# Performance work log

Measured on AMD Instinct MI355X. Metric: run time of the kernel, lower is better.

## Reference

```python
import jax, jax.numpy as jnp
import numpy as np
from jax import lax

B, L, V, D, E, K, H, IMG = 256, 64, 32000, 1024, 8, 2, 512, 128


def setup_inputs() -> dict:
    key = jax.random.key(0)
    ks = jax.random.split(key, 24)
    n = lambda k, sh, s=0.02: (jax.random.normal(k, sh, jnp.float32) * s)
    return {
        "img": jax.random.normal(ks[0], (B, 3, IMG, IMG), jnp.float32),
        "tokens": jax.random.randint(ks[1], (B, L), 0, V),
        "mask": jnp.ones((B, L), jnp.int32),
        # image encoder convs (OIHW) + biases
        "cw1": n(ks[2], (32, 3, 3, 3)), "cb1": jnp.zeros((32,), jnp.float32),
        "cw2": n(ks[3], (64, 32, 3, 3)), "cb2": jnp.zeros((64,), jnp.float32),
        "cw3": n(ks[4], (128, 64, 3, 3)), "cb3": jnp.zeros((128,), jnp.float32),
        "cw4": n(ks[5], (256, 128, 3, 3)), "cb4": jnp.zeros((256,), jnp.float32),
        "enc_proj_w": n(ks[6], (256, D)), "enc_proj_b": jnp.zeros((D,), jnp.float32),
        # text encoder
        "embed": n(ks[7], (V, D)),
        # gate
        "gate_w": n(ks[8], (D, E)), "gate_b": jnp.zeros((E,), jnp.float32),
        # experts (stacked): y = relu(x@W1+b1)@W2+b2
        "exp_w1": n(ks[9], (E, D, H)), "exp_b1": jnp.zeros((E, H), jnp.float32),
        "exp_w2": n(ks[10], (E, H, D)), "exp_b2": jnp.zeros((E, D), jnp.float32),
        # contrastive projections (bias=False)
        "img_proj_w": n(ks[11], (D, D)),
        "txt_proj_w": n(ks[12], (D, D)),
        "logit_scale": jnp.log(jnp.float32(1.0 / 0.07)),
    }


def _conv(x, w, b, stride):
    y = lax.conv_general_dilated(x, w, (stride, stride), 'SAME',
                                 dimension_numbers=('NCHW', 'OIHW', 'NCHW'))
    return y + b[None, :, None, None]


def _img_encode(img, cw1, cb1, cw2, cb2, cw3, cb3, cw4, cb4, pw, pb):
    h = jax.nn.relu(_conv(img, cw1, cb1, 1))
    h = jax.nn.relu(_conv(h, cw2, cb2, 2))
    h = jax.nn.relu(_conv(h, cw3, cb3, 2))
    h = jax.nn.relu(_conv(h, cw4, cb4, 2))
    h = h.mean(axis=(2, 3))  # [B, 256]
    return h @ pw + pb


def _txt_encode(tokens, mask, embed):
    x = embed[tokens]                      # [B, L, D]
    m = mask[..., None].astype(jnp.float32)
    return (x * m).sum(axis=1) / jnp.maximum(m.sum(axis=1), 1.0)


def _moe(x, gate_w, gate_b, w1, b1, w2, b2):
    logits = x @ gate_w + gate_b                       # [B, E]
    probs = jax.nn.softmax(logits, axis=-1)
    topk_vals, topk_idx = lax.top_k(probs, K)
    w = topk_vals / (topk_vals.sum(axis=-1, keepdims=True) + 1e-9)  # [B, K]
    # dense expert compute (same math as the per-expert masked loop)
    h = jax.nn.relu(jnp.einsum('bd,edh->ebh', x, w1) + b1[:, None, :])
    y = jnp.einsum('ebh,ehd->ebd', h, w2) + b2[:, None, :]          # [E, B, D]
    y = jnp.transpose(y, (1, 0, 2))                                  # [B, E, D]
    sel = jnp.take_along_axis(y, topk_idx[:, :, None], axis=1)       # [B, K, D]
    out = (sel * w[:, :, None]).sum(axis=1)
    # F.kl_div(mean_probs.log(), uniform, reduction='batchmean')
    mp = probs.mean(axis=0)
    u = 1.0 / E
    aux = jnp.sum(u * (jnp.log(jnp.float32(u)) - jnp.log(mp))) / E
    return out, aux


def _normalize(x):
    return x / jnp.maximum(jnp.linalg.norm(x, axis=-1, keepdims=True), 1e-12)


def reference(img, tokens, mask, cw1, cb1, cw2, cb2, cw3, cb3, cw4, cb4,
              enc_proj_w, enc_proj_b, embed, gate_w, gate_b,
              exp_w1, exp_b1, exp_w2, exp_b2, img_proj_w, txt_proj_w, logit_scale):
    h_img = _img_encode(img, cw1, cb1, cw2, cb2, cw3, cb3, cw4, cb4, enc_proj_w, enc_proj_b)
    h_txt = _txt_encode(tokens, mask, embed)
    z_img, aux_img = _moe(h_img, gate_w, gate_b, exp_w1, exp_b1, exp_w2, exp_b2)
    z_txt, aux_txt = _moe(h_txt, gate_w, gate_b, exp_w1, exp_b1, exp_w2, exp_b2)
    e_img = _normalize(z_img @ img_proj_w)
    e_txt = _normalize(z_txt @ txt_proj_w)
    scale = jnp.minimum(jnp.exp(logit_scale), 100.0)
    logits_per_img = scale * (e_img @ e_txt.T)
    logits_per_txt = logits_per_img.T
    aux_loss = (aux_img + aux_txt) * 0.5
    return logits_per_img, logits_per_txt, aux_loss
```

## Files before the change

### kernel.cpp

```cpp
#include <hip/hip_runtime.h>
#include <hip/hip_bf16.h>
#include <math.h>

#define BATCH 256
#define CHUNK 32
#define NCHUNK (BATCH / CHUNK)
#define ECAP 256
#define NEXP 16

__global__ __launch_bounds__(256) void conv1_tiled(const float* __restrict__ in,
                                                   const float* __restrict__ w,
                                                   const float* __restrict__ bias,
                                                   float* __restrict__ out) {
  const int t = threadIdx.x;
  const int bc = blockIdx.x;
  const int quad = bc & 3;
  const int co = (bc >> 2) & 31;
  const int b = bc >> 7;
  const int tile = quad * 256 + t;
  const int tr = tile >> 4;
  const int tc = tile & 15;
  const int oh0 = tr * 2, ow0 = tc * 8;

  float wk[3][9];
#pragma unroll
  for (int ci = 0; ci < 3; ++ci)
#pragma unroll
    for (int k = 0; k < 9; ++k) wk[ci][k] = w[(co * 3 + ci) * 9 + k];

  const float bv = bias[co];
  float acc[2][8];
#pragma unroll
  for (int r = 0; r < 2; ++r)
#pragma unroll
    for (int c = 0; c < 8; ++c) acc[r][c] = bv;

  const float* __restrict__ ip = in + (size_t)b * 3 * 128 * 128;
#pragma unroll
  for (int ci = 0; ci < 3; ++ci) {
    const float* __restrict__ p = ip + ci * 128 * 128;
    float x[4][10];
#pragma unroll
    for (int r = 0; r < 4; ++r) {
      const int ih = oh0 - 1 + r;
      if (ih >= 0 && ih < 128) {
        const float* rowp = p + ih * 128 + ow0;
        x[r][0] = (ow0 > 0) ? rowp[-1] : 0.f;
        const float4 f0 = *(const float4*)(rowp);
        const float4 f1 = *(const float4*)(rowp + 4);
        x[r][1] = f0.x; x[r][2] = f0.y; x[r][3] = f0.z; x[r][4] = f0.w;
        x[r][5] = f1.x; x[r][6] = f1.y; x[r][7] = f1.z; x[r][8] = f1.w;
        x[r][9] = (ow0 + 8 < 128) ? rowp[8] : 0.f;
      } else {
#pragma unroll
        for (int q = 0; q < 10; ++q) x[r][q] = 0.f;
      }
    }
#pragma unroll
    for (int kh = 0; kh < 3; ++kh)
#pragma unroll
      for (int kw = 0; kw < 3; ++kw) {
        const float wv = wk[ci][kh * 3 + kw];
#pragma unroll
        for (int r = 0; r < 2; ++r)
#pragma unroll
          for (int c = 0; c < 8; ++c)
            acc[r][c] = fmaf(x[r + kh][c + kw], wv, acc[r][c]);
      }
  }
  float* __restrict__ op = out + (((size_t)b * 32 + co) * 128 + oh0) * 128 + ow0;
#pragma unroll
  for (int r = 0; r < 2; ++r)
#pragma unroll
    for (int c = 0; c < 8; ++c) op[r * 128 + c] = fmaxf(acc[r][c], 0.f);
}

template<int CIN, int HIN, int WIN, int HOUT, int WOUT, int COUT, int TH, int TW, int SLABS>
__global__ __launch_bounds__(256) void conv_s2_r4(const float* __restrict__ in,
                                                  const float* __restrict__ w,
                                                  const float* __restrict__ bias,
                                                  float* __restrict__ out) {
  constexpr int TPR = WOUT / TW;
  constexpr int TT = (HOUT / TH) * TPR;
  static_assert(TT == 64 * SLABS, "tile count mismatch");
  constexpr int GPI = (SLABS == 4) ? (COUT / 4) : (COUT / 16);
  const int wave = threadIdx.x >> 6;
  const int lane = threadIdx.x & 63;
  const int b = blockIdx.x / GPI;
  const int r = blockIdx.x % GPI;
  int cg, slab;
  if (SLABS == 4) { cg = r; slab = wave; }
  else           { cg = r * 4 + wave; slab = 0; }
  const int co0 = __builtin_amdgcn_readfirstlane(cg * 4);
  const int tile = slab * 64 + lane;
  const int tr = tile / TPR, tc = tile % TPR;
  const int oh0 = tr * TH, ow0 = tc * TW;
  const int ih0 = oh0 * 2, iw0 = ow0 * 2;

  const float* __restrict__ ip = in + (size_t)b * CIN * HIN * WIN + ih0 * WIN + iw0;
  const float* __restrict__ wp = w + (size_t)co0 * CIN * 9;

  float bv[4];
#pragma unroll
  for (int j = 0; j < 4; ++j) bv[j] = bias[co0 + j];
  float acc[4][TH][TW];
#pragma unroll
  for (int j = 0; j < 4; ++j)
#pragma unroll
    for (int rr = 0; rr < TH; ++rr)
#pragma unroll
      for (int c = 0; c < TW; ++c) acc[j][rr][c] = bv[j];

  for (int ci = 0; ci < CIN; ++ci) {
    float wk[4][9];
#pragma unroll
    for (int j = 0; j < 4; ++j)
#pragma unroll
      for (int k = 0; k < 9; ++k) wk[j][k] = wp[((size_t)j * CIN + ci) * 9 + k];

    float x[2 * TH + 1][2 * TW + 1];
    const float* __restrict__ rp = ip + (size_t)ci * HIN * WIN;
#pragma unroll
    for (int rr = 0; rr < 2 * TH + 1; ++rr) {
      const int ih = ih0 + rr;
      if (ih < HIN) {
        const float* rowp = rp + rr * WIN;
#pragma unroll
        for (int q = 0; q < (2 * TW) / 4; ++q) {
          const float4 f = *(const float4*)(rowp + q * 4);
          x[rr][q * 4 + 0] = f.x; x[rr][q * 4 + 1] = f.y;
          x[rr][q * 4 + 2] = f.z; x[rr][q * 4 + 3] = f.w;
        }
        x[rr][2 * TW] = (iw0 + 2 * TW < WIN) ? rowp[2 * TW] : 0.f;
      } else {
#pragma unroll
        for (int q = 0; q < 2 * TW + 1; ++q) x[rr][q] = 0.f;
      }
    }
#pragma unroll
    for (int kh = 0; kh < 3; ++kh)
#pragma unroll
      for (int kw = 0; kw < 3; ++kw) {
#pragma unroll
        for (int j = 0; j < 4; ++j) {
          const float wv = wk[j][kh * 3 + kw];
#pragma unroll
          for (int rr = 0; rr < TH; ++rr)
#pragma unroll
            for (int c = 0; c < TW; ++c)
              acc[j][rr][c] = fmaf(x[2 * rr + kh][2 * c + kw], wv, acc[j][rr][c]);
        }
      }
  }
#pragma unroll
  for (int j = 0; j < 4; ++j) {
    float* __restrict__ op = out + (((size_t)b * COUT + co0 + j) * HOUT + oh0) * WOUT + ow0;
#pragma unroll
    for (int rr = 0; rr < TH; ++rr)
#pragma unroll
      for (int c = 0; c < TW; ++c) op[rr * WOUT + c] = fmaxf(acc[j][rr][c], 0.f);
  }
}

__global__ __launch_bounds__(64) void pool_mean(const float* __restrict__ in,
                                                float* __restrict__ out) {
  const int bc = blockIdx.x;
  const float* p = in + (size_t)bc * 256;
  float s = p[threadIdx.x] + p[threadIdx.x + 64] + p[threadIdx.x + 128] + p[threadIdx.x + 192];
#pragma unroll
  for (int off = 32; off; off >>= 1) s += __shfl_down(s, off);
  if (threadIdx.x == 0) out[bc] = s * (1.f / 256.f);
}

__global__ __launch_bounds__(256) void enc_proj(const float* __restrict__ pooled,
                                                const float* __restrict__ W,
                                                const float* __restrict__ bias,
                                                float* __restrict__ out) {
  __shared__ float xs[256];
  const int b = blockIdx.x;
  const int t = threadIdx.x;
  xs[t] = pooled[b * 256 + t];
  __syncthreads();
#pragma unroll
  for (int dd = 0; dd < 4; ++dd) {
    const int d = t + dd * 256;
    float acc = bias[d];
    for (int i = 0; i < 256; ++i) acc = fmaf(xs[i], W[i * 1024 + d], acc);
    out[b * 1024 + d] = acc;
  }
}

__global__ __launch_bounds__(256) void txt_encode(const int* __restrict__ tokens,
                                                  const int* __restrict__ mask,
                                                  const float* __restrict__ embed,
                                                  float* __restrict__ out) {
  __shared__ int toks[64];
  __shared__ float ms[64];
  const int b = blockIdx.x;
  const int t = threadIdx.x;
  if (t < 64) {
    toks[t] = tokens[b * 64 + t];
    ms[t] = (float)mask[b * 64 + t];
  }
  __syncthreads();
  float denom = 0.f;
  for (int l = 0; l < 64; ++l) denom += ms[l];
  denom = fmaxf(denom, 1.f);
  const float inv = 1.f / denom;
#pragma unroll
  for (int dd = 0; dd < 4; ++dd) {
    const int d = t + dd * 256;
    float acc = 0.f;
    for (int l = 0; l < 64; ++l)
      acc = fmaf(embed[(size_t)toks[l] * 1024 + d], ms[l], acc);
    out[b * 1024 + d] = acc * inv;
  }
}

__global__ __launch_bounds__(64) void zero_cnt(int* __restrict__ cnt) {
  if (threadIdx.x < NEXP) cnt[threadIdx.x] = 0;
}

__global__ __launch_bounds__(256) void gate_topk(const float* __restrict__ x,
                                                 const float* __restrict__ gw,
                                                 const float* __restrict__ gb,
                                                 float* __restrict__ probs_out,
                                                 float* __restrict__ sel_w,
                                                 int* __restrict__ slot_of,
                                                 int* __restrict__ cnt,
                                                 int* __restrict__ slot_tok,
                                                 int emod_base) {
  const int b = blockIdx.x;
  __shared__ float part[256];
  __shared__ float logits[8];
  const int e = threadIdx.x & 7;
  const int ch = threadIdx.x >> 3;
  float acc = 0.f;
  for (int d = ch * 32; d < ch * 32 + 32; ++d)
    acc = fmaf(x[b * 1024 + d], gw[d * 8 + e], acc);
  part[threadIdx.x] = acc;
  __syncthreads();
  if (threadIdx.x < 8) {
    float s = gb[threadIdx.x];
    for (int c = 0; c < 32; ++c) s += part[c * 8 + threadIdx.x];
    logits[threadIdx.x] = s;
  }
  __syncthreads();
  if (threadIdx.x == 0) {
    float mx = logits[0];
    for (int i = 1; i < 8; ++i) mx = fmaxf(mx, logits[i]);
    float pe[8], sum = 0.f;
    for (int i = 0; i < 8; ++i) { pe[i] = expf(logits[i] - mx); sum += pe[i]; }
    const float inv = 1.f / sum;
    int i0 = 0;
    for (int i = 1; i < 8; ++i) if (pe[i] > pe[i0]) i0 = i;
    int i1 = (i0 == 0) ? 1 : 0;
    for (int i = 0; i < 8; ++i) { if (i == i0) continue; if (pe[i] > pe[i1]) i1 = i; }
    for (int i = 0; i < 8; ++i) probs_out[b * 8 + i] = pe[i] * inv;
    const float v0 = pe[i0] * inv, v1 = pe[i1] * inv;
    const float wsum = v0 + v1 + 1e-9f;
    const int sel[2] = {i0, i1};
    const float sw[2] = {v0 / wsum, v1 / wsum};
#pragma unroll
    for (int k = 0; k < 2; ++k) {
      const int ve = emod_base + sel[k];
      const int slot = atomicAdd(&cnt[ve], 1);
      slot_tok[ve * ECAP + slot] = b;
      slot_of[b * 2 + k] = ve * ECAP + slot;
      sel_w[b * 2 + k] = sw[k];
    }
  }
}

__global__ __launch_bounds__(256) void moe_ffn1(const float* __restrict__ h_img,
                                                const float* __restrict__ h_txt,
                                                const int* __restrict__ cnt,
                                                const int* __restrict__ slot_tok,
                                                const float* __restrict__ W1,
                                                const float* __restrict__ B1,
                                                float* __restrict__ hbuf) {
  const int ve = blockIdx.x >> 5;
  const int rem = blockIdx.x & 31;
  const int tchunk = rem >> 2;
  const int nchunk = rem & 3;
  const int tbase = tchunk * 32;
  const int scnt = cnt[ve];
  if (tbase >= scnt) return;
  const int n0 = nchunk * 128;
  const int e = ve & 7;
  const float* __restrict__ xsrc = (ve < 8) ? h_img : h_txt;
  const float* __restrict__ w1 = W1 + (size_t)e * 1024 * 512;

  __shared__ float xs[32][36];
  __shared__ float ws[32][128];

  const int tid = threadIdx.x;
  const int tokr = tid >> 3, kq = tid & 7;
  const int sidx = tbase + tokr;
  const int tok = (sidx < scnt) ? slot_tok[ve * ECAP + sidx] : 0;
  const int tn = tid & 31, tt = tid >> 5;
  const int n4 = tn * 4, t4 = tt * 4;

  float acc[4][4] = {};
  for (int k0 = 0; k0 < 1024; k0 += 32) {
    const float4 xv = *(const float4*)(xsrc + (size_t)tok * 1024 + k0 + kq * 4);
    float4 wv[4];
#pragma unroll
    for (int i = 0; i < 4; ++i) {
      const int idx = tid + i * 256;
      const int kk = idx >> 5, nq = idx & 31;
      wv[i] = *(const float4*)(w1 + (size_t)(k0 + kk) * 512 + n0 + nq * 4);
    }
    __syncthreads();
    xs[kq * 4 + 0][tokr] = xv.x; xs[kq * 4 + 1][tokr] = xv.y;
    xs[kq * 4 + 2][tokr] = xv.z; xs[kq * 4 + 3][tokr] = xv.w;
#pragma unroll
    for (int i = 0; i < 4; ++i) {
      const int idx = tid + i * 256;
      const int kk = idx >> 5, nq = idx & 31;
      *(float4*)&ws[kk][nq * 4] = wv[i];
    }
    __syncthreads();
#pragma unroll
    for (int k = 0; k < 32; ++k) {
      const float4 xr = *(const float4*)&xs[k][t4];
      const float4 wr = *(const float4*)&ws[k][n4];
      const float xa[4] = {xr.x, xr.y, xr.z, xr.w};
      const float wa[4] = {wr.x, wr.y, wr.z, wr.w};
#pragma unroll
      for (int ti = 0; ti < 4; ++ti)
#pragma unroll
        for (int ni = 0; ni < 4; ++ni)
          acc[ti][ni] = fmaf(xa[ti], wa[ni], acc[ti][ni]);
    }
  }
#pragma unroll
  for (int ti = 0; ti < 4; ++ti) {
    float* hp = hbuf + ((size_t)ve * ECAP + tbase + t4 + ti) * 512 + n0 + n4;
#pragma unroll
    for (int ni = 0; ni < 4; ++ni)
      hp[ni] = fmaxf(acc[ti][ni] + B1[e * 512 + n0 + n4 + ni], 0.f);
  }
}

__global__ __launch_bounds__(256) void moe_ffn2(const float* __restrict__ hbuf,
                                                const int* __restrict__ cnt,
                                                const float* __restrict__ W2,
                                                const float* __restrict__ B2,
                                                float* __restrict__ ybuf) {
  const int ve = blockIdx.x >> 6;
  const int rem = blockIdx.x & 63;
  const int tchunk = rem >> 3;
  const int nchunk = rem & 7;
  const int tbase = tchunk * 32;
  const int scnt = cnt[ve];
  if (tbase >= scnt) return;
  const int n0 = nchunk * 128;
  const int e = ve & 7;
  const float* __restrict__ w2 = W2 + (size_t)e * 512 * 1024;

  __shared__ float hs[32][36];
  __shared__ float ws[32][128];

  const int tid = threadIdx.x;
  const int tokr = tid >> 3, kq = tid & 7;
  const int tn = tid & 31, tt = tid >> 5;
  const int n4 = tn * 4, t4 = tt * 4;

  float acc[4][4] = {};
  for (int k0 = 0; k0 < 512; k0 += 32) {
    const float4 hv = *(const float4*)(hbuf + ((size_t)ve * ECAP + tbase + tokr) * 512 + k0 + kq * 4);
    float4 wv[4];
#pragma unroll
    for (int i = 0; i < 4; ++i) {
      const int idx = tid + i * 256;
      const int kk = idx >> 5, nq = idx & 31;
      wv[i] = *(const float4*)(w2 + (size_t)(k0 + kk) * 1024 + n0 + nq * 4);
    }
    __syncthreads();
    hs[kq * 4 + 0][tokr] = hv.x; hs[kq * 4 + 1][tokr] = hv.y;
    hs[kq * 4 + 2][tokr] = hv.z; hs[kq * 4 + 3][tokr] = hv.w;
#pragma unroll
    for (int i = 0; i < 4; ++i) {
      const int idx = tid + i * 256;
      const int kk = idx >> 5, nq = idx & 31;
      *(float4*)&ws[kk][nq * 4] = wv[i];
    }
    __syncthreads();
#pragma unroll
    for (int k = 0; k < 32; ++k) {
      const float4 xr = *(const float4*)&hs[k][t4];
      const float4 wr = *(const float4*)&ws[k][n4];
      const float xa[4] = {xr.x, xr.y, xr.z, xr.w};
      const float wa[4] = {wr.x, wr.y, wr.z, wr.w};
#pragma unroll
      for (int ti = 0; ti < 4; ++ti)
#pragma unroll
        for (int ni = 0; ni < 4; ++ni)
          acc[ti][ni] = fmaf(xa[ti], wa[ni], acc[ti][ni]);
    }
  }
#pragma unroll
  for (int ti = 0; ti < 4; ++ti) {
    float* yp = ybuf + ((size_t)ve * ECAP + tbase + t4 + ti) * 1024 + n0 + n4;
#pragma unroll
    for (int ni = 0; ni < 4; ++ni)
      yp[ni] = acc[ti][ni] + B2[e * 1024 + n0 + n4 + ni];
  }
}

__global__ __launch_bounds__(256) void moe_combine(const float* __restrict__ ybuf,
                                                   const int* __restrict__ slot_of,
                                                   const float* __restrict__ sel_w,
                                                   float* __restrict__ z_img,
                                                   float* __restrict__ z_txt) {
  const int bb = blockIdx.x;
  const int mod = bb >> 8;
  const int b = bb & 255;
  const int s0 = slot_of[bb * 2], s1 = slot_of[bb * 2 + 1];
  const float w0 = sel_w[bb * 2], w1 = sel_w[bb * 2 + 1];
  float* __restrict__ zp = (mod ? z_txt : z_img) + (size_t)b * 1024;
  const float* __restrict__ y0 = ybuf + (size_t)s0 * 1024;
  const float* __restrict__ y1 = ybuf + (size_t)s1 * 1024;
  const int t = threadIdx.x;
#pragma unroll
  for (int dd = 0; dd < 4; ++dd) {
    const int d = t + dd * 256;
    zp[d] = w0 * y0[d] + w1 * y1[d];
  }
}

__global__ __launch_bounds__(256) void proj_norm(const float* __restrict__ z,
                                                 const float* __restrict__ W,
                                                 float* __restrict__ e_out) {
  const int b = blockIdx.x;
  const int t = threadIdx.x;
  __shared__ float xs[1024];
  __shared__ float red[256];
#pragma unroll
  for (int i = 0; i < 4; ++i) xs[t + i * 256] = z[b * 1024 + t + i * 256];
  __syncthreads();
  float p[4];
  float ss = 0.f;
#pragma unroll
  for (int dd = 0; dd < 4; ++dd) {
    const int d = t + dd * 256;
    float acc = 0.f;
    for (int i = 0; i < 1024; ++i) acc = fmaf(xs[i], W[i * 1024 + d], acc);
    p[dd] = acc;
    ss += acc * acc;
  }
  red[t] = ss;
  __syncthreads();
  for (int off = 128; off; off >>= 1) {
    if (t < off) red[t] += red[t + off];
    __syncthreads();
  }
  const float inv = 1.f / fmaxf(sqrtf(red[0]), 1e-12f);
#pragma unroll
  for (int dd = 0; dd < 4; ++dd) e_out[b * 1024 + t + dd * 256] = p[dd] * inv;
}

__global__ __launch_bounds__(256) void clip_logits(const float* __restrict__ ei,
                                                   const float* __restrict__ et,
                                                   const float* __restrict__ logit_scale,
                                                   float* __restrict__ out_pi,
                                                   float* __restrict__ out_pt) {
  const int i = blockIdx.x;
  const int j = threadIdx.x;
  __shared__ float row[1024];
#pragma unroll
  for (int c = 0; c < 4; ++c) row[j + c * 256] = ei[i * 1024 + j + c * 256];
  __syncthreads();
  float acc = 0.f;
  const float* __restrict__ tp = et + (size_t)j * 1024;
  for (int d = 0; d < 1024; ++d) acc = fmaf(row[d], tp[d], acc);
  const float s = fminf(expf(logit_scale[0]), 100.f);
  const float v = s * acc;
  out_pi[i * 256 + j] = v;
  out_pt[j * 256 + i] = v;
}

__global__ __launch_bounds__(256) void aux_kernel(const float* __restrict__ probs_i,
                                                  const float* __restrict__ probs_t,
                                                  float* __restrict__ out_aux) {
  __shared__ float red[256];
  const int t = threadIdx.x;
  float aux[2];
  for (int m = 0; m < 2; ++m) {
    const float* __restrict__ p = m ? probs_t : probs_i;
    float a = 0.f;
    for (int e = 0; e < 8; ++e) {
      red[t] = p[t * 8 + e];
      __syncthreads();
      for (int off = 128; off; off >>= 1) {
        if (t < off) red[t] += red[t + off];
        __syncthreads();
      }
      const float mp = red[0] * (1.f / 256.f);
      a += 0.125f * (logf(0.125f) - logf(mp));
      __syncthreads();
    }
    aux[m] = a * 0.125f;
  }
  if (t == 0) out_aux[0] = 0.5f * (aux[0] + aux[1]);
}

extern "C" void kernel_launch(void* const* d_in, const int* in_sizes, int n_in,
                              void* d_out, int out_size, void* d_ws, size_t ws_size,
                              hipStream_t stream) {
  const float* img        = (const float*)d_in[0];
  const int*   tokens     = (const int*)d_in[1];
  const int*   mask       = (const int*)d_in[2];
  const float* cw1        = (const float*)d_in[3];
  const float* cb1        = (const float*)d_in[4];
  const float* cw2        = (const float*)d_in[5];
  const float* cb2        = (const float*)d_in[6];
  const float* cw3        = (const float*)d_in[7];
  const float* cb3        = (const float*)d_in[8];
  const float* cw4        = (const float*)d_in[9];
  const float* cb4        = (const float*)d_in[10];
  const float* enc_proj_w = (const float*)d_in[11];
  const float* enc_proj_b = (const float*)d_in[12];
  const float* embed      = (const float*)d_in[13];
  const float* gate_w     = (const float*)d_in[14];
  const float* gate_b     = (const float*)d_in[15];
  const float* exp_w1     = (const float*)d_in[16];
  const float* exp_b1     = (const float*)d_in[17];
  const float* exp_w2     = (const float*)d_in[18];
  const float* exp_b2     = (const float*)d_in[19];
  const float* img_proj_w = (const float*)d_in[20];
  const float* txt_proj_w = (const float*)d_in[21];
  const float* logit_sc   = (const float*)d_in[22];
  float* out = (float*)d_out;

  float* bufA   = (float*)d_ws;
  float* bufB   = bufA + 16777216;
  float* pooled = bufB + 8388608;
  float* h_img  = pooled + 65536;
  float* h_txt  = h_img + 262144;
  float* z_img  = h_txt + 262144;
  float* z_txt  = z_img + 262144;
  float* e_img  = z_txt + 262144;
  float* e_txt  = e_img + 262144;
  float* probs_img = e_txt + 262144;
  float* probs_txt = probs_img + 2048;
  float* sel_w  = probs_txt + 2048;
  int* slot_of  = (int*)(sel_w + 1024);
  int* slot_tok = slot_of + 1024;
  int* cnt      = slot_tok + 4096;
  float* hbuf = bufA;
  float* ybuf = bufA + (size_t)NEXP * ECAP * 512;

  zero_cnt<<<1, 64, 0, stream>>>(cnt);

  for (int c = 0; c < NCHUNK; ++c) {
    const float* imgc = img + (size_t)c * CHUNK * 3 * 128 * 128;
    conv1_tiled<<<CHUNK * 32 * 4, 256, 0, stream>>>(imgc, cw1, cb1, bufA);
    conv_s2_r4<32, 128, 128, 64, 64, 64, 2, 8, 4>
        <<<CHUNK * 16, 256, 0, stream>>>(bufA, cw2, cb2, bufB);
    conv_s2_r4<64, 64, 64, 32, 32, 128, 2, 8, 1>
        <<<CHUNK * 8, 256, 0, stream>>>(bufB, cw3, cb3, bufA);
    conv_s2_r4<128, 32, 32, 16, 16, 256, 2, 2, 1>
        <<<CHUNK * 16, 256, 0, stream>>>(bufA, cw4, cb4, bufB);
    pool_mean<<<CHUNK * 256, 64, 0, stream>>>(bufB, pooled + (size_t)c * CHUNK * 256);
  }
  enc_proj<<<BATCH, 256, 0, stream>>>(pooled, enc_proj_w, enc_proj_b, h_img);

  txt_encode<<<BATCH, 256, 0, stream>>>(tokens, mask, embed, h_txt);

  gate_topk<<<BATCH, 256, 0, stream>>>(h_img, gate_w, gate_b, probs_img,
                                       sel_w, slot_of, cnt, slot_tok, 0);
  gate_topk<<<BATCH, 256, 0, stream>>>(h_txt, gate_w, gate_b, probs_txt,
                                       sel_w + 512, slot_of + 512, cnt, slot_tok, 8);
  moe_ffn1<<<NEXP * 32, 256, 0, stream>>>(h_img, h_txt, cnt, slot_tok,
                                          exp_w1, exp_b1, hbuf);
  moe_ffn2<<<NEXP * 64, 256, 0, stream>>>(hbuf, cnt, exp_w2, exp_b2, ybuf);
  moe_combine<<<512, 256, 0, stream>>>(ybuf, slot_of, sel_w, z_img, z_txt);

  proj_norm<<<BATCH, 256, 0, stream>>>(z_img, img_proj_w, e_img);
  proj_norm<<<BATCH, 256, 0, stream>>>(z_txt, txt_proj_w, e_txt);
  clip_logits<<<BATCH, 256, 0, stream>>>(e_img, e_txt, logit_sc, out, out + 65536);
  aux_kernel<<<1, 256, 0, stream>>>(probs_img, probs_txt, out + 131072);
}
```

Baseline: 4.138 ms.

## Fuse conv4 with pooling, tile projection GEMM, and size image chunks to workspace

Conv4 now sums its ReLU outputs inside the kernel with wave shuffles, so the full conv4 activation map and the separate pool kernel are no longer needed. The per-row projection, which streamed the whole 1024x1024 weight for every sample, becomes an LDS-tiled GEMM followed by a separate row-normalization kernel covering both modalities. Image chunk size is chosen from the available workspace to cut the number of launches. The logits dot product also uses float4 loads. The cost is an extra launch for normalization and less parallelism per conv4 block.

After: 3.875 ms. -6.4%, faster.

```diff
diff --git a/kernel.cpp b/kernel.cpp
--- a/kernel.cpp
+++ b/kernel.cpp
@@ -3,8 +3,6 @@
 #include <math.h>
 
 #define BATCH 256
-#define CHUNK 32
-#define NCHUNK (BATCH / CHUNK)
 #define ECAP 256
 #define NEXP 16
 
@@ -162,14 +160,87 @@
   }
 }
 
-__global__ __launch_bounds__(64) void pool_mean(const float* __restrict__ in,
-                                                float* __restrict__ out) {
-  const int bc = blockIdx.x;
-  const float* p = in + (size_t)bc * 256;
-  float s = p[threadIdx.x] + p[threadIdx.x + 64] + p[threadIdx.x + 128] + p[threadIdx.x + 192];
-#pragma unroll
-  for (int off = 32; off; off >>= 1) s += __shfl_down(s, off);
-  if (threadIdx.x == 0) out[bc] = s * (1.f / 256.f);
+__global__ __launch_bounds__(256) void conv4_pool(const float* __restrict__ in,
+                                                  const float* __restrict__ w,
+                                                  const float* __restrict__ bias,
+                                                  float* __restrict__ pooled) {
+  constexpr int CIN = 128, HIN = 32, WIN = 32;
+  const int wave = threadIdx.x >> 6;
+  const int lane = threadIdx.x & 63;
+  const int b = blockIdx.x >> 4;
+  const int r = blockIdx.x & 15;
+  const int cg = r * 4 + wave;
+  const int co0 = __builtin_amdgcn_readfirstlane(cg * 4);
+  const int tr = lane >> 3, tc = lane & 7;
+  const int oh0 = tr * 2, ow0 = tc * 2;
+  const int ih0 = oh0 * 2, iw0 = ow0 * 2;
+
+  const float* __restrict__ ip = in + (size_t)b * CIN * HIN * WIN + ih0 * WIN + iw0;
+  const float* __restrict__ wp = w + (size_t)co0 * CIN * 9;
+
+  float bv[4];
+#pragma unroll
+  for (int j = 0; j < 4; ++j) bv[j] = bias[co0 + j];
+  float acc[4][2][2];
+#pragma unroll
+  for (int j = 0; j < 4; ++j)
+#pragma unroll
+    for (int rr = 0; rr < 2; ++rr)
+#pragma unroll
+      for (int c = 0; c < 2; ++c) acc[j][rr][c] = bv[j];
+
+  for (int ci = 0; ci < CIN; ++ci) {
+    float wk[4][9];
+#pragma unroll
+    for (int j = 0; j < 4; ++j)
+#pragma unroll
+      for (int k = 0; k < 9; ++k) wk[j][k] = wp[((size_t)j * CIN + ci) * 9 + k];
+
+    float x[5][5];
+    const float* __restrict__ rp = ip + (size_t)ci * HIN * WIN;
+#pragma unroll
+    for (int rr = 0; rr < 5; ++rr) {
+      const int ih = ih0 + rr;
+      if (ih < HIN) {
+        const float* rowp = rp + rr * WIN;
+        const float4 f = *(const float4*)(rowp);
+        x[rr][0] = f.x; x[rr][1] = f.y; x[rr][2] = f.z; x[rr][3] = f.w;
+        x[rr][4] = (iw0 + 4 < WIN) ? rowp[4] : 0.f;
+      } else {
+#pragma unroll
+        for (int q = 0; q < 5; ++q) x[rr][q] = 0.f;
+      }
+    }
+#pragma unroll
+    for (int kh = 0; kh < 3; ++kh)
+#pragma unroll
+      for (int kw = 0; kw < 3; ++kw) {
+#pragma unroll
+        for (int j = 0; j < 4; ++j) {
+          const float wv = wk[j][kh * 3 + kw];
+#pragma unroll
+          for (int rr = 0; rr < 2; ++rr)
+#pragma unroll
+            for (int c = 0; c < 2; ++c)
+              acc[j][rr][c] = fmaf(x[2 * rr + kh][2 * c + kw], wv, acc[j][rr][c]);
+        }
+      }
+  }
+  float s[4];
+#pragma unroll
+  for (int j = 0; j < 4; ++j)
+    s[j] = fmaxf(acc[j][0][0], 0.f) + fmaxf(acc[j][0][1], 0.f) +
+           fmaxf(acc[j][1][0], 0.f) + fmaxf(acc[j][1][1], 0.f);
+#pragma unroll
+  for (int off = 32; off; off >>= 1) {
+#pragma unroll
+    for (int j = 0; j < 4; ++j) s[j] += __shfl_down(s[j], off);
+  }
+  if (lane == 0) {
+#pragma unroll
+    for (int j = 0; j < 4; ++j)
+      pooled[b * 256 + co0 + j] = s[j] * (1.f / 256.f);
+  }
 }
 
 __global__ __launch_bounds__(256) void enc_proj(const float* __restrict__ pooled,
@@ -430,26 +501,78 @@
   }
 }
 
-__global__ __launch_bounds__(256) void proj_norm(const float* __restrict__ z,
-                                                 const float* __restrict__ W,
-                                                 float* __restrict__ e_out) {
+__global__ __launch_bounds__(256) void proj_gemm(const float* __restrict__ z_img,
+                                                 const float* __restrict__ z_txt,
+                                                 const float* __restrict__ Wimg,
+                                                 const float* __restrict__ Wtxt,
+                                                 float* __restrict__ e_img,
+                                                 float* __restrict__ e_txt) {
+  const int bid = blockIdx.x;
+  const int mod = bid >> 6;
+  const int tchunk = (bid >> 3) & 7;
+  const int nchunk = bid & 7;
+  const int tbase = tchunk * 32;
+  const int n0 = nchunk * 128;
+  const float* __restrict__ x = mod ? z_txt : z_img;
+  const float* __restrict__ W = mod ? Wtxt : Wimg;
+  float* __restrict__ P = mod ? e_txt : e_img;
+
+  __shared__ float xs[32][36];
+  __shared__ float ws[32][128];
+
+  const int tid = threadIdx.x;
+  const int tokr = tid >> 3, kq = tid & 7;
+  const int tn = tid & 31, tt = tid >> 5;
+  const int n4 = tn * 4, t4 = tt * 4;
+
+  float acc[4][4] = {};
+  for (int k0 = 0; k0 < 1024; k0 += 32) {
+    const float4 xv = *(const float4*)(x + (size_t)(tbase + tokr) * 1024 + k0 + kq * 4);
+    float4 wv[4];
+#pragma unroll
+    for (int i = 0; i < 4; ++i) {
+      const int idx = tid + i * 256;
+      const int kk = idx >> 5, nq = idx & 31;
+      wv[i] = *(const float4*)(W + (size_t)(k0 + kk) * 1024 + n0 + nq * 4);
+    }
+    __syncthreads();
+    xs[kq * 4 + 0][tokr] = xv.x; xs[kq * 4 + 1][tokr] = xv.y;
+    xs[kq * 4 + 2][tokr] = xv.z; xs[kq * 4 + 3][tokr] = xv.w;
+#pragma unroll
+    for (int i = 0; i < 4; ++i) {
+      const int idx = tid + i * 256;
+      const int kk = idx >> 5, nq = idx & 31;
+      *(float4*)&ws[kk][nq * 4] = wv[i];
+    }
+    __syncthreads();
+#pragma unroll
+    for (int k = 0; k < 32; ++k) {
+      const float4 xr = *(const float4*)&xs[k][t4];
+      const float4 wr = *(const float4*)&ws[k][n4];
+      const float xa[4] = {xr.x, xr.y, xr.z, xr.w};
+      const float wa[4] = {wr.x, wr.y, wr.z, wr.w};
+#pragma unroll
+      for (int ti = 0; ti < 4; ++ti)
+#pragma unroll
+        for (int ni = 0; ni < 4; ++ni)
+          acc[ti][ni] = fmaf(xa[ti], wa[ni], acc[ti][ni]);
+    }
+  }
+#pragma unroll
+  for (int ti = 0; ti < 4; ++ti) {
+    float* pp = P + (size_t)(tbase + t4 + ti) * 1024 + n0 + n4;
+#pragma unroll
+    for (int ni = 0; ni < 4; ++ni) pp[ni] = acc[ti][ni];
+  }
+}
+
+__global__ __launch_bounds__(256) void norm_rows(float* __restrict__ p) {
   const int b = blockIdx.x;
   const int t = threadIdx.x;
-  __shared__ float xs[1024];
   __shared__ float red[256];
-#pragma unroll
-  for (int i = 0; i < 4; ++i) xs[t + i * 256] = z[b * 1024 + t + i * 256];
-  __syncthreads();
-  float p[4];
-  float ss = 0.f;
-#pragma unroll
-  for (int dd = 0; dd < 4; ++dd) {
-    const int d = t + dd * 256;
-    float acc = 0.f;
-    for (int i = 0; i < 1024; ++i) acc = fmaf(xs[i], W[i * 1024 + d], acc);
-    p[dd] = acc;
-    ss += acc * acc;
-  }
+  float* __restrict__ row = p + (size_t)b * 1024;
+  float4 v = *(const float4*)(row + t * 4);
+  float ss = v.x * v.x + v.y * v.y + v.z * v.z + v.w * v.w;
   red[t] = ss;
   __syncthreads();
   for (int off = 128; off; off >>= 1) {
@@ -457,8 +580,8 @@
     __syncthreads();
   }
   const float inv = 1.f / fmaxf(sqrtf(red[0]), 1e-12f);
-#pragma unroll
-  for (int dd = 0; dd < 4; ++dd) e_out[b * 1024 + t + dd * 256] = p[dd] * inv;
+  v.x *= inv; v.y *= inv; v.z *= inv; v.w *= inv;
+  *(float4*)(row + t * 4) = v;
 }
 
 __global__ __launch_bounds__(256) void clip_logits(const float* __restrict__ ei,
@@ -473,8 +596,15 @@
   for (int c = 0; c < 4; ++c) row[j + c * 256] = ei[i * 1024 + j + c * 256];
   __syncthreads();
   float acc = 0.f;
-  const float* __restrict__ tp = et + (size_t)j * 1024;
-  for (int d = 0; d < 1024; ++d) acc = fmaf(row[d], tp[d], acc);
+  const float4* __restrict__ tp = (const float4*)(et + (size_t)j * 1024);
+  for (int d = 0; d < 256; ++d) {
+    const float4 tv = tp[d];
+    const float4 rv = *(const float4*)&row[d * 4];
+    acc = fmaf(rv.x, tv.x, acc);
+    acc = fmaf(rv.y, tv.y, acc);
+    acc = fmaf(rv.z, tv.z, acc);
+    acc = fmaf(rv.w, tv.w, acc);
+  }
   const float s = fminf(expf(logit_scale[0]), 100.f);
   const float v = s * acc;
   out_pi[i * 256 + j] = v;
@@ -534,9 +664,17 @@
   const float* logit_sc   = (const float*)d_in[22];
   float* out = (float*)d_out;
 
+  const size_t tail_floats = 1648656;
+  int chunk = 32;
+  for (int c = 256; c >= 32; c >>= 1) {
+    const size_t need = ((size_t)c * 786432 + tail_floats) * 4;
+    if (need <= ws_size) { chunk = c; break; }
+  }
+  const int nchunk = BATCH / chunk;
+
   float* bufA   = (float*)d_ws;
-  float* bufB   = bufA + 16777216;
-  float* pooled = bufB + 8388608;
+  float* bufB   = bufA + (size_t)chunk * 524288;
+  float* pooled = bufB + (size_t)chunk * 262144;
   float* h_img  = pooled + 65536;
   float* h_txt  = h_img + 262144;
   float* z_img  = h_txt + 262144;
@@ -554,16 +692,15 @@
 
   zero_cnt<<<1, 64, 0, stream>>>(cnt);
 
-  for (int c = 0; c < NCHUNK; ++c) {
-    const float* imgc = img + (size_t)c * CHUNK * 3 * 128 * 128;
-    conv1_tiled<<<CHUNK * 32 * 4, 256, 0, stream>>>(imgc, cw1, cb1, bufA);
+  for (int c = 0; c < nchunk; ++c) {
+    const float* imgc = img + (size_t)c * chunk * 3 * 128 * 128;
+    conv1_tiled<<<chunk * 32 * 4, 256, 0, stream>>>(imgc, cw1, cb1, bufA);
     conv_s2_r4<32, 128, 128, 64, 64, 64, 2, 8, 4>
-        <<<CHUNK * 16, 256, 0, stream>>>(bufA, cw2, cb2, bufB);
+        <<<chunk * 16, 256, 0, stream>>>(bufA, cw2, cb2, bufB);
     conv_s2_r4<64, 64, 64, 32, 32, 128, 2, 8, 1>
-        <<<CHUNK * 8, 256, 0, stream>>>(bufB, cw3, cb3, bufA);
-    conv_s2_r4<128, 32, 32, 16, 16, 256, 2, 2, 1>
-        <<<CHUNK * 16, 256, 0, stream>>>(bufA, cw4, cb4, bufB);
-    pool_mean<<<CHUNK * 256, 64, 0, stream>>>(bufB, pooled + (size_t)c * CHUNK * 256);
+        <<<chunk * 8, 256, 0, stream>>>(bufB, cw3, cb3, bufA);
+    conv4_pool<<<chunk * 16, 256, 0, stream>>>(bufA, cw4, cb4,
+                                               pooled + (size_t)c * chunk * 256);
   }
   enc_proj<<<BATCH, 256, 0, stream>>>(pooled, enc_proj_w, enc_proj_b, h_img);
 
@@ -578,8 +715,8 @@
   moe_ffn2<<<NEXP * 64, 256, 0, stream>>>(hbuf, cnt, exp_w2, exp_b2, ybuf);
   moe_combine<<<512, 256, 0, stream>>>(ybuf, slot_of, sel_w, z_img, z_txt);
 
-  proj_norm<<<BATCH, 256, 0, stream>>>(z_img, img_proj_w, e_img);
-  proj_norm<<<BATCH, 256, 0, stream>>>(z_txt, txt_proj_w, e_txt);
+  proj_gemm<<<128, 256, 0, stream>>>(z_img, z_txt, img_proj_w, txt_proj_w, e_img, e_txt);
+  norm_rows<<<512, 256, 0, stream>>>(e_img);
   clip_logits<<<BATCH, 256, 0, stream>>>(e_img, e_txt, logit_sc, out, out + 65536);
   aux_kernel<<<1, 256, 0, stream>>>(probs_img, probs_txt, out + 131072);
 }
```
